# Kernel optimization log

Hardware: AMD Instinct MI355X
Metric: run time of the kernel (lower is better)

Reference implementation:

```python
import jax, jax.numpy as jnp
import numpy as np

B, P, C = 64, 196, 768   # batch, num_patches, hidden_size
HS = 384                 # hidden_s (token-mixing hidden dim)
NG = 8                   # num_grids
GMIN, GMAX = -1.0, 1.0


def _rbf(x):
    # fast-KAN radial basis: exp(-((x - grid_i)/denom)^2), grid over [GMIN, GMAX]
    grid = jnp.linspace(GMIN, GMAX, NG).astype(x.dtype)
    denom = (GMAX - GMIN) / (NG - 1)
    return jnp.exp(-jnp.square((x[..., None] - grid) / denom))  # [..., din, NG]


def _kan_linear(x, spline_w, base_w, base_b):
    # x: [..., din]; spline_w: [dout, din*NG]; base_w: [dout, din]; base_b: [dout]
    basis = _rbf(x).reshape(*x.shape[:-1], -1)          # [..., din*NG]
    out = basis @ spline_w.T                            # spline term (no bias)
    out = out + jax.nn.silu(x) @ base_w.T + base_b      # base update term
    return out


def setup_inputs() -> dict:
    key = jax.random.key(0)
    ks = jax.random.split(key, 5)
    s = 0.1  # spline_weight_init_scale
    return {
        "x": jax.random.normal(ks[0], (B, P, C), jnp.float32),
        "fc1_spline_w": jax.random.normal(ks[1], (HS, P * NG), jnp.float32) * (s / np.sqrt(P * NG)),
        "fc1_base_w": jax.random.normal(ks[2], (HS, P), jnp.float32) / np.sqrt(P),
        "fc1_base_b": jnp.zeros((HS,), jnp.float32),
        "fc2_spline_w": jax.random.normal(ks[3], (P, HS * NG), jnp.float32) * (s / np.sqrt(HS * NG)),
        "fc2_base_w": jax.random.normal(ks[4], (P, HS), jnp.float32) / np.sqrt(HS),
        "fc2_base_b": jnp.zeros((P,), jnp.float32),
    }


def reference(x, fc1_spline_w, fc1_base_w, fc1_base_b,
              fc2_spline_w, fc2_base_w, fc2_base_b):
    skip_param = 1.0
    # token mixing: permute so KANLinear acts over the patch axis
    h = jnp.swapaxes(x, 1, 2)                                   # [B, C, P]
    h = _kan_linear(h, fc1_spline_w, fc1_base_w, fc1_base_b)    # [B, C, HS]
    # dropout p=0 -> identity; the two intermediate permutes cancel
    h = _kan_linear(h, fc2_spline_w, fc2_base_w, fc2_base_b)    # [B, C, P]
    out = jnp.swapaxes(h, 1, 2)                                 # [B, P, C]
    return out + skip_param * x
```

## Files before the change

### kernel.cpp

```cpp
#include <hip/hip_runtime.h>
#include <cstdint>

#define B_  64
#define P_  196
#define C_  768
#define HS_ 384
#define M_  49152
#define RT_ 96
#define NB_ (M_ / RT_)

#define NC1 13
#define KT1 111
#define NT1 12
#define NC2 24
#define KT2 216
#define NT2 7

#define H1_ELEMS  ((size_t)M_ * HS_)
#define W1P_ELEMS ((size_t)KT1 * NT1 * 512)
#define W2P_ELEMS ((size_t)KT2 * NT2 * 512)

typedef __attribute__((ext_vector_type(8)))  short short8;
typedef __attribute__((ext_vector_type(16))) float f32x16;

#define MFMA(w, a, c) __builtin_amdgcn_mfma_f32_32x32x16_bf16((w), (a), (c), 0, 0, 0)

static __device__ __forceinline__ float bf2f(unsigned short u) {
    union { unsigned int i; float f; } v; v.i = ((unsigned int)u) << 16; return v.f;
}
static __device__ __forceinline__ unsigned short f2bf_rne(float f) {
    union { float f; unsigned int i; } v; v.f = f;
    unsigned int r = v.i + 0x7FFFu + ((v.i >> 16) & 1u);
    return (unsigned short)(r >> 16);
}
static __device__ __forceinline__ unsigned int pack2(float a, float b) {
    unsigned int ua = __float_as_uint(a) + 0x8000u;
    unsigned int ub = __float_as_uint(b) + 0x8000u;
    return __builtin_amdgcn_perm(ub, ua, 0x07060302u);
}
static __device__ __forceinline__ short8 rbf8(float s) {
    const float Rr = 1.2011224087864498f;
    const float Aa = 4.2039284307525743f;
    float t1 = __builtin_fmaf(Aa, s, Aa);
    union { short8 s8; unsigned int u[4]; } r;
#pragma unroll
    for (int q = 0; q < 4; q++) {
        float u0 = t1 - (float)(2 * q) * Rr;
        float u1 = t1 - (float)(2 * q + 1) * Rr;
        r.u[q] = pack2(__builtin_amdgcn_exp2f(-u0 * u0),
                       __builtin_amdgcn_exp2f(-u1 * u1));
    }
    return r.s8;
}
static __device__ __forceinline__ unsigned int silu2(float a, float b) {
    const float L2E = 1.4426950408889634f;
    float fa = a * __builtin_amdgcn_rcpf(1.f + __builtin_amdgcn_exp2f(-L2E * a));
    float fb = b * __builtin_amdgcn_rcpf(1.f + __builtin_amdgcn_exp2f(-L2E * b));
    return pack2(fa, fb);
}

__global__ void pack_w_kernel(const float* __restrict__ w1s,
                              const float* __restrict__ w1b,
                              const float* __restrict__ w2s,
                              const float* __restrict__ w2b,
                              unsigned short* __restrict__ w1p,
                              unsigned short* __restrict__ w2p) {
    size_t idx = (size_t)blockIdx.x * 256 + threadIdx.x;
    if (idx < W1P_ELEMS) {
        int j    = idx & 7;
        int lane = (idx >> 3) & 63;
        int lin  = idx >> 9;
        int nt   = lin % NT1;
        int tt   = lin / NT1;
        int cc   = (tt < 108) ? tt / 9 : 12;
        int kk   = (tt < 108) ? tt % 9 : (tt - 108);
        int ktl  = (cc < 12) ? kk : ((kk < 2) ? kk : 8);
        int n = nt * 32 + (lane & 31);
        int khalf = lane >> 5;
        float v = 0.f;
        if (ktl < 8) {
            int p = cc * 16 + ktl * 2 + khalf;
            if (p < P_) v = w1s[(size_t)n * 1568 + p * 8 + j];
        } else {
            int p = cc * 16 + khalf * 8 + j;
            if (p < P_) v = w1b[(size_t)n * 196 + p];
        }
        w1p[idx] = f2bf_rne(v);
    } else {
        size_t idx2 = idx - W1P_ELEMS;
        if (idx2 < W2P_ELEMS) {
            int j    = idx2 & 7;
            int lane = (idx2 >> 3) & 63;
            int lin  = idx2 >> 9;
            int nt   = lin % NT2;
            int tt   = lin / NT2;
            int cc   = tt / 9;
            int ktl  = tt % 9;
            int n = nt * 32 + (lane & 31);
            int khalf = lane >> 5;
            float v = 0.f;
            if (n < P_) {
                if (ktl < 8) {
                    int s = cc * 16 + ktl * 2 + khalf;
                    v = w2s[(size_t)n * 3072 + s * 8 + j];
                } else {
                    int s = cc * 16 + khalf * 8 + j;
                    v = w2b[(size_t)n * 384 + s];
                }
            }
            w2p[idx2] = f2bf_rne(v);
        }
    }
}

#define TS_  1536
#define FB_  (9 * TS_)


__global__ __launch_bounds__(256, 2)
void fc1_kernel(const float* __restrict__ x,
                const unsigned short* __restrict__ w1p,
                const float* __restrict__ b1,
                unsigned short* __restrict__ h1t) {
    __shared__ __align__(16) unsigned short frag[2 * FB_];
    int blk = blockIdx.x;
    int tid = threadIdx.x;
    int b   = blk >> 3;
    int c0  = (blk & 7) * RT_;
    const float* xb = x + (size_t)b * (P_ * C_);

    int colA = tid & 63, scA = tid >> 6;
    int colB = 64 + (tid & 31), scB = tid >> 5;
    int pbase_rbfA  = ((colA >> 5) << 9) + (colA & 31) * 8;
    int pbase_rbfB  = 1024 + (colB & 31) * 8;
    int pbase_siluA = 8 * TS_ + ((colA >> 5) << 9) + ((scA >> 1) << 8) + (colA & 31) * 8 + (scA & 1) * 4;
    int pbase_siluB = 8 * TS_ + 1024 + ((scB >> 2) << 8) + (colB & 31) * 8 + (scB & 3) * 2;

    int wave = tid >> 6, lane = tid & 63;
    int l31 = lane & 31, half = lane >> 5;
    int nt0 = wave * 3;

    f32x16 acc[3][3];
#pragma unroll
    for (int rt = 0; rt < 3; rt++)
#pragma unroll
        for (int nt = 0; nt < 3; nt++)
#pragma unroll
            for (int i = 0; i < 16; i++) acc[rt][nt][i] = 0.f;

    const short8* wp = (const short8*)w1p;
    short8 wbuf[2][3];

    auto wload = [&](int d, const short8* wt0, int kk) {
        const short8* wt = wt0 + (size_t)kk * (NT1 * 64);
        wbuf[d][0] = wt[0]; wbuf[d][1] = wt[64]; wbuf[d][2] = wt[128];
    };
    auto do_mfma = [&](short8 w0, short8 w1, short8 w2,
                       short8 a0, short8 a1, short8 a2) {
        acc[0][0] = MFMA(w0, a0, acc[0][0]); acc[1][0] = MFMA(w0, a1, acc[1][0]); acc[2][0] = MFMA(w0, a2, acc[2][0]);
        acc[0][1] = MFMA(w1, a0, acc[0][1]); acc[1][1] = MFMA(w1, a1, acc[1][1]); acc[2][1] = MFMA(w1, a2, acc[2][1]);
        acc[0][2] = MFMA(w2, a0, acc[0][2]); acc[1][2] = MFMA(w2, a1, acc[1][2]); acc[2][2] = MFMA(w2, a2, acc[2][2]);
    };
    auto produce = [&](int fb, const float (&ra)[4], const float (&rb2)[2]) {
#pragma unroll
        for (int i = 0; i < 4; i++) {
            int sl = scA * 4 + i;
            *(short8*)&frag[fb + (sl >> 1) * TS_ + ((sl & 1) << 8) + pbase_rbfA] = rbf8(ra[i]);
        }
#pragma unroll
        for (int i = 0; i < 2; i++) {
            int sl = scB * 2 + i;
            *(short8*)&frag[fb + (sl >> 1) * TS_ + ((sl & 1) << 8) + pbase_rbfB] = rbf8(rb2[i]);
        }
        uint2 sv;
        sv.x = silu2(ra[0], ra[1]);
        sv.y = silu2(ra[2], ra[3]);
        *(uint2*)&frag[fb + pbase_siluA] = sv;
        *(unsigned int*)&frag[fb + pbase_siluB] = silu2(rb2[0], rb2[1]);
    };
    auto body = [&](int cc, const float (&rbPA)[4], const float (&rbPB)[2],
                    float (&rbLA)[4], float (&rbLB)[2]) {
        const short8* wt0 = wp + ((size_t)(cc * 9) * NT1 + nt0) * 64 + lane;
        wload(0, wt0, 0); wload(1, wt0, 1);
        int fbP = ((cc + 1) & 1) * FB_;
        const unsigned short* fg = &frag[(cc & 1) * FB_];
        short8 a0 = *(const short8*)&fg[lane * 8];
        short8 a1 = *(const short8*)&fg[512 + lane * 8];
        short8 a2 = *(const short8*)&fg[1024 + lane * 8];
#pragma unroll
        for (int kk = 0; kk < 9; kk++) {
            short8 na0, na1, na2;
            if (kk < 8) {
                na0 = *(const short8*)&fg[(kk + 1) * TS_ + lane * 8];
                na1 = *(const short8*)&fg[(kk + 1) * TS_ + 512 + lane * 8];
                na2 = *(const short8*)&fg[(kk + 1) * TS_ + 1024 + lane * 8];
            }
            short8 w0 = wbuf[kk & 1][0], w1 = wbuf[kk & 1][1], w2 = wbuf[kk & 1][2];
            if (kk < 7) wload(kk & 1, wt0, kk + 2);
            if (kk < 4) {
                int sl = scA * 4 + kk;
                *(short8*)&frag[fbP + (sl >> 1) * TS_ + ((sl & 1) << 8) + pbase_rbfA] = rbf8(rbPA[kk]);
            } else if (kk == 4) {
#pragma unroll
                for (int i = 0; i < 2; i++) {
                    int sl = scB * 2 + i;
                    *(short8*)&frag[fbP + (sl >> 1) * TS_ + ((sl & 1) << 8) + pbase_rbfB] = rbf8(rbPB[i]);
                }
            } else if (kk == 5) {
                uint2 sv;
                sv.x = silu2(rbPA[0], rbPA[1]);
                sv.y = silu2(rbPA[2], rbPA[3]);
                *(uint2*)&frag[fbP + pbase_siluA] = sv;
                *(unsigned int*)&frag[fbP + pbase_siluB] = silu2(rbPB[0], rbPB[1]);
            } else if (kk == 6) {
#pragma unroll
                for (int i = 0; i < 2; i++) {
                    int p = (cc + 2) * 16 + scA * 4 + i;
                    p = (p < P_) ? p : (P_ - 1);
                    rbLA[i] = xb[(size_t)p * C_ + c0 + colA];
                }
            } else if (kk == 7) {
#pragma unroll
                for (int i = 2; i < 4; i++) {
                    int p = (cc + 2) * 16 + scA * 4 + i;
                    p = (p < P_) ? p : (P_ - 1);
                    rbLA[i] = xb[(size_t)p * C_ + c0 + colA];
                }
            } else {
#pragma unroll
                for (int i = 0; i < 2; i++) {
                    int p = (cc + 2) * 16 + scB * 2 + i;
                    p = (p < P_) ? p : (P_ - 1);
                    rbLB[i] = xb[(size_t)p * C_ + c0 + colB];
                }
            }
            do_mfma(w0, w1, w2, a0, a1, a2);
            if (kk < 8) { a0 = na0; a1 = na1; a2 = na2; }
        }
        __syncthreads();
    };

    float rbA_A[4], rbB_A[4], rbA_B[2], rbB_B[2];
#pragma unroll
    for (int i = 0; i < 4; i++) {
        rbA_A[i] = xb[(size_t)(scA * 4 + i) * C_ + c0 + colA];
        rbB_A[i] = xb[(size_t)(16 + scA * 4 + i) * C_ + c0 + colA];
    }
#pragma unroll
    for (int i = 0; i < 2; i++) {
        rbA_B[i] = xb[(size_t)(scB * 2 + i) * C_ + c0 + colB];
        rbB_B[i] = xb[(size_t)(16 + scB * 2 + i) * C_ + c0 + colB];
    }
    produce(0, rbA_A, rbA_B);
    __syncthreads();

    for (int c2 = 0; c2 < 6; c2++) {
        body(2 * c2,     rbB_A, rbB_B, rbA_A, rbA_B);
        body(2 * c2 + 1, rbA_A, rbA_B, rbB_A, rbB_B);
    }
    {
        const short8* wt0 = wp + ((size_t)108 * NT1 + nt0) * 64 + lane;
        wload(0, wt0, 0); wload(1, wt0, 1);
        const unsigned short* fg = &frag[0];
#pragma unroll
        for (int kk = 0; kk < 3; kk++) {
            short8 w0 = wbuf[kk & 1][0], w1 = wbuf[kk & 1][1], w2 = wbuf[kk & 1][2];
            if (kk == 0) wload(0, wt0, 2);
            int ktl = (kk < 2) ? kk : 8;
            short8 a0 = *(const short8*)&fg[ktl * TS_ + lane * 8];
            short8 a1 = *(const short8*)&fg[ktl * TS_ + 512 + lane * 8];
            short8 a2 = *(const short8*)&fg[ktl * TS_ + 1024 + lane * 8];
            do_mfma(w0, w1, w2, a0, a1, a2);
        }
    }

#pragma unroll
    for (int nt = 0; nt < 3; nt++) {
        int n0 = (nt0 + nt) * 32 + 4 * half;
#pragma unroll
        for (int reg = 0; reg < 16; reg++) {
            int n = n0 + (reg & 3) + 8 * (reg >> 2);
            float bv = b1[n];
#pragma unroll
            for (int rt = 0; rt < 3; rt++) {
                h1t[(size_t)n * M_ + blk * RT_ + rt * 32 + l31] = f2bf_rne(acc[rt][nt][reg] + bv);
            }
        }
    }
}

__global__ __launch_bounds__(256, 2)
void fc2_kernel(const unsigned short* __restrict__ h1t,
                const unsigned short* __restrict__ w2p,
                const float* __restrict__ b2,
                const float* __restrict__ x,
                float* __restrict__ out) {
    __shared__ __align__(16) unsigned short frag[2 * FB_];
    int blk = blockIdx.x;
    int tid = threadIdx.x;
    int rbase = blk * RT_;

    int colA = tid & 63, scA = tid >> 6;
    int colB = 64 + (tid & 31), scB = tid >> 5;
    int pbase_rbfA  = ((colA >> 5) << 9) + (colA & 31) * 8;
    int pbase_rbfB  = 1024 + (colB & 31) * 8;
    int pbase_siluA = 8 * TS_ + ((colA >> 5) << 9) + ((scA >> 1) << 8) + (colA & 31) * 8 + (scA & 1) * 4;
    int pbase_siluB = 8 * TS_ + 1024 + ((scB >> 2) << 8) + (colB & 31) * 8 + (scB & 3) * 2;

    int wave = tid >> 6, lane = tid & 63;
    int l31 = lane & 31, half = lane >> 5;
    int nt0 = wave * 2;
    int ntn = (wave < 3) ? 2 : 1;
    int off1 = (ntn > 1) ? 64 : 0;

    f32x16 acc[3][2];
#pragma unroll
    for (int rt = 0; rt < 3; rt++)
#pragma unroll
        for (int nt = 0; nt < 2; nt++)
#pragma unroll
            for (int i = 0; i < 16; i++) acc[rt][nt][i] = 0.f;

    const short8* wp = (const short8*)w2p;
    short8 wbuf[2][2];

    auto wload = [&](int d, const short8* wt0, int kk) {
        const short8* wt = wt0 + (size_t)kk * (NT2 * 64);
        wbuf[d][0] = wt[0]; wbuf[d][1] = wt[off1];
    };
    auto do_mfma = [&](short8 w0, short8 w1, short8 a0, short8 a1, short8 a2) {
        acc[0][0] = MFMA(w0, a0, acc[0][0]); acc[1][0] = MFMA(w0, a1, acc[1][0]); acc[2][0] = MFMA(w0, a2, acc[2][0]);
        if (ntn == 2) {
            acc[0][1] = MFMA(w1, a0, acc[0][1]); acc[1][1] = MFMA(w1, a1, acc[1][1]); acc[2][1] = MFMA(w1, a2, acc[2][1]);
        }
    };
    auto produce = [&](int fb, const unsigned short (&ra)[4], const unsigned short (&rb2)[2]) {
        float v0 = bf2f(ra[0]), v1 = bf2f(ra[1]), v2 = bf2f(ra[2]), v3 = bf2f(ra[3]);
        float u0 = bf2f(rb2[0]), u1 = bf2f(rb2[1]);
        float vv[4] = {v0, v1, v2, v3};
#pragma unroll
        for (int i = 0; i < 4; i++) {
            int sl = scA * 4 + i;
            *(short8*)&frag[fb + (sl >> 1) * TS_ + ((sl & 1) << 8) + pbase_rbfA] = rbf8(vv[i]);
        }
        float uu[2] = {u0, u1};
#pragma unroll
        for (int i = 0; i < 2; i++) {
            int sl = scB * 2 + i;
            *(short8*)&frag[fb + (sl >> 1) * TS_ + ((sl & 1) << 8) + pbase_rbfB] = rbf8(uu[i]);
        }
        uint2 sv;
        sv.x = silu2(v0, v1);
        sv.y = silu2(v2, v3);
        *(uint2*)&frag[fb + pbase_siluA] = sv;
        *(unsigned int*)&frag[fb + pbase_siluB] = silu2(u0, u1);
    };
    auto body = [&](int cc, const unsigned short (&rbPA)[4], const unsigned short (&rbPB)[2],
                    unsigned short (&rbLA)[4], unsigned short (&rbLB)[2]) {
        bool doProd = (cc + 1 < NC2);
        const short8* wt0 = wp + ((size_t)(cc * 9) * NT2 + nt0) * 64 + lane;
        wload(0, wt0, 0); wload(1, wt0, 1);
        int fbP = ((cc + 1) & 1) * FB_;
        const unsigned short* fg = &frag[(cc & 1) * FB_];
        short8 a0 = *(const short8*)&fg[lane * 8];
        short8 a1 = *(const short8*)&fg[512 + lane * 8];
        short8 a2 = *(const short8*)&fg[1024 + lane * 8];
#pragma unroll
        for (int kk = 0; kk < 9; kk++) {
            short8 na0, na1, na2;
            if (kk < 8) {
                na0 = *(const short8*)&fg[(kk + 1) * TS_ + lane * 8];
                na1 = *(const short8*)&fg[(kk + 1) * TS_ + 512 + lane * 8];
                na2 = *(const short8*)&fg[(kk + 1) * TS_ + 1024 + lane * 8];
            }
            short8 w0 = wbuf[kk & 1][0], w1 = wbuf[kk & 1][1];
            if (kk < 7) wload(kk & 1, wt0, kk + 2);
            if (kk < 4) {
                if (doProd) {
                    int sl = scA * 4 + kk;
                    *(short8*)&frag[fbP + (sl >> 1) * TS_ + ((sl & 1) << 8) + pbase_rbfA] =
                        rbf8(bf2f(rbPA[kk]));
                }
            } else if (kk == 4) {
                if (doProd) {
#pragma unroll
                    for (int i = 0; i < 2; i++) {
                        int sl = scB * 2 + i;
                        *(short8*)&frag[fbP + (sl >> 1) * TS_ + ((sl & 1) << 8) + pbase_rbfB] =
                            rbf8(bf2f(rbPB[i]));
                    }
                }
            } else if (kk == 5) {
                if (doProd) {
                    uint2 sv;
                    sv.x = silu2(bf2f(rbPA[0]), bf2f(rbPA[1]));
                    sv.y = silu2(bf2f(rbPA[2]), bf2f(rbPA[3]));
                    *(uint2*)&frag[fbP + pbase_siluA] = sv;
                    *(unsigned int*)&frag[fbP + pbase_siluB] = silu2(bf2f(rbPB[0]), bf2f(rbPB[1]));
                }
            } else if (kk == 6) {
#pragma unroll
                for (int i = 0; i < 2; i++) {
                    int s = (cc + 2) * 16 + scA * 4 + i;
                    s = (s < HS_) ? s : (HS_ - 1);
                    rbLA[i] = h1t[(size_t)s * M_ + rbase + colA];
                }
            } else if (kk == 7) {
#pragma unroll
                for (int i = 2; i < 4; i++) {
                    int s = (cc + 2) * 16 + scA * 4 + i;
                    s = (s < HS_) ? s : (HS_ - 1);
                    rbLA[i] = h1t[(size_t)s * M_ + rbase + colA];
                }
            } else {
#pragma unroll
                for (int i = 0; i < 2; i++) {
                    int s = (cc + 2) * 16 + scB * 2 + i;
                    s = (s < HS_) ? s : (HS_ - 1);
                    rbLB[i] = h1t[(size_t)s * M_ + rbase + colB];
                }
            }
            do_mfma(w0, w1, a0, a1, a2);
            if (kk < 8) { a0 = na0; a1 = na1; a2 = na2; }
        }
        __syncthreads();
    };

    unsigned short rbA_A[4], rbB_A[4], rbA_B[2], rbB_B[2];
#pragma unroll
    for (int i = 0; i < 4; i++) {
        rbA_A[i] = h1t[(size_t)(scA * 4 + i) * M_ + rbase + colA];
        rbB_A[i] = h1t[(size_t)(16 + scA * 4 + i) * M_ + rbase + colA];
    }
#pragma unroll
    for (int i = 0; i < 2; i++) {
        rbA_B[i] = h1t[(size_t)(scB * 2 + i) * M_ + rbase + colB];
        rbB_B[i] = h1t[(size_t)(16 + scB * 2 + i) * M_ + rbase + colB];
    }
    produce(0, rbA_A, rbA_B);
    __syncthreads();

    for (int c2 = 0; c2 < 12; c2++) {
        body(2 * c2,     rbB_A, rbB_B, rbA_A, rbA_B);
        body(2 * c2 + 1, rbA_A, rbA_B, rbB_A, rbB_B);
    }

    int b = blk >> 3;
    int c0 = (blk & 7) * RT_;
#pragma unroll
    for (int nt = 0; nt < 2; nt++) {
        if (nt < ntn) {
            int p0 = (nt0 + nt) * 32 + 4 * half;
#pragma unroll
            for (int reg = 0; reg < 16; reg++) {
                int p = p0 + (reg & 3) + 8 * (reg >> 2);
                if (p < P_) {
                    float bv = b2[p];
#pragma unroll
                    for (int rt = 0; rt < 3; rt++) {
                        size_t off = ((size_t)b * P_ + p) * C_ + c0 + rt * 32 + l31;
                        out[off] = acc[rt][nt][reg] + bv + x[off];
                    }
                }
            }
        }
    }
}

extern "C" void kernel_launch(void* const* d_in, const int* in_sizes, int n_in,
                              void* d_out, int out_size, void* d_ws, size_t ws_size,
                              hipStream_t stream) {
    const float* x   = (const float*)d_in[0];
    const float* w1s = (const float*)d_in[1];
    const float* w1b = (const float*)d_in[2];
    const float* b1  = (const float*)d_in[3];
    const float* w2s = (const float*)d_in[4];
    const float* w2b = (const float*)d_in[5];
    const float* b2  = (const float*)d_in[6];
    float* out = (float*)d_out;

    unsigned short* h1t = (unsigned short*)d_ws;
    unsigned short* w1p = h1t + H1_ELEMS;
    unsigned short* w2p = w1p + W1P_ELEMS;

    int pack_blocks = (int)((W1P_ELEMS + W2P_ELEMS) / 256);
    pack_w_kernel<<<pack_blocks, 256, 0, stream>>>(w1s, w1b, w2s, w2b, w1p, w2p);
    fc1_kernel<<<NB_, 256, 0, stream>>>(x, w1p, b1, h1t);
    fc2_kernel<<<NB_, 256, 0, stream>>>(h1t, w2p, b2, x, out);
}
```

Before: 248.5 us.

## Build RBF/SiLU MFMA operands in registers instead of via LDS staging

Both KAN GEMM kernels drop the shared-memory fragment buffers and the per-chunk __syncthreads. Each wave now loads the x/h1 values it needs straight from global memory and computes the RBF and SiLU bf16 operands in registers, right before each MFMA. This removes LDS writes and reads and the block barriers. In exchange, every wave recomputes the basis for all row tiles instead of sharing that work across the block, which raises redundant global loads and VALU work. fc1 also gives up its cross-chunk prefetch of x, since it now loads x at the start of each chunk.

```diff
diff --git a/kernel.cpp b/kernel.cpp
--- a/kernel.cpp
+++ b/kernel.cpp
@@ -113,31 +113,21 @@
     }
 }
 
-#define TS_  1536
-#define FB_  (9 * TS_)
-
 
 __global__ __launch_bounds__(256, 2)
 void fc1_kernel(const float* __restrict__ x,
                 const unsigned short* __restrict__ w1p,
                 const float* __restrict__ b1,
                 unsigned short* __restrict__ h1t) {
-    __shared__ __align__(16) unsigned short frag[2 * FB_];
     int blk = blockIdx.x;
     int tid = threadIdx.x;
     int b   = blk >> 3;
     int c0  = (blk & 7) * RT_;
     const float* xb = x + (size_t)b * (P_ * C_);
 
-    int colA = tid & 63, scA = tid >> 6;
-    int colB = 64 + (tid & 31), scB = tid >> 5;
-    int pbase_rbfA  = ((colA >> 5) << 9) + (colA & 31) * 8;
-    int pbase_rbfB  = 1024 + (colB & 31) * 8;
-    int pbase_siluA = 8 * TS_ + ((colA >> 5) << 9) + ((scA >> 1) << 8) + (colA & 31) * 8 + (scA & 1) * 4;
-    int pbase_siluB = 8 * TS_ + 1024 + ((scB >> 2) << 8) + (colB & 31) * 8 + (scB & 3) * 2;
-
     int wave = tid >> 6, lane = tid & 63;
-    int l31 = lane & 31, half = lane >> 5;
+    int l31 = lane & 31, khalf = lane >> 5;
+    int half = khalf;
     int nt0 = wave * 3;
 
     f32x16 acc[3][3];
@@ -147,9 +137,13 @@
         for (int nt = 0; nt < 3; nt++)
 #pragma unroll
             for (int i = 0; i < 16; i++) acc[rt][nt][i] = 0.f;
+
+    const float* pr0 = xb + (size_t)khalf * C_ + c0 + l31;
+    const float* pm0 = xb + (size_t)(1 + 7 * khalf) * C_ + c0 + l31;
 
     const short8* wp = (const short8*)w1p;
     short8 wbuf[2][3];
+    float xr[3][8], xm[3][4];
 
     auto wload = [&](int d, const short8* wt0, int kk) {
         const short8* wt = wt0 + (size_t)kk * (NT1 * 64);
@@ -161,116 +155,81 @@
         acc[0][1] = MFMA(w1, a0, acc[0][1]); acc[1][1] = MFMA(w1, a1, acc[1][1]); acc[2][1] = MFMA(w1, a2, acc[2][1]);
         acc[0][2] = MFMA(w2, a0, acc[0][2]); acc[1][2] = MFMA(w2, a1, acc[1][2]); acc[2][2] = MFMA(w2, a2, acc[2][2]);
     };
-    auto produce = [&](int fb, const float (&ra)[4], const float (&rb2)[2]) {
-#pragma unroll
-        for (int i = 0; i < 4; i++) {
-            int sl = scA * 4 + i;
-            *(short8*)&frag[fb + (sl >> 1) * TS_ + ((sl & 1) << 8) + pbase_rbfA] = rbf8(ra[i]);
-        }
-#pragma unroll
-        for (int i = 0; i < 2; i++) {
-            int sl = scB * 2 + i;
-            *(short8*)&frag[fb + (sl >> 1) * TS_ + ((sl & 1) << 8) + pbase_rbfB] = rbf8(rb2[i]);
-        }
-        uint2 sv;
-        sv.x = silu2(ra[0], ra[1]);
-        sv.y = silu2(ra[2], ra[3]);
-        *(uint2*)&frag[fb + pbase_siluA] = sv;
-        *(unsigned int*)&frag[fb + pbase_siluB] = silu2(rb2[0], rb2[1]);
-    };
-    auto body = [&](int cc, const float (&rbPA)[4], const float (&rbPB)[2],
-                    float (&rbLA)[4], float (&rbLB)[2]) {
+    auto loadx = [&](int cc) {
+#pragma unroll
+        for (int rt = 0; rt < 3; rt++) {
+            const float* r = pr0 + rt * 32;
+            const float* m = pm0 + rt * 32;
+#pragma unroll
+            for (int i = 0; i < 8; i++) xr[rt][i] = r[(size_t)(cc * 16 + 2 * i) * C_];
+#pragma unroll
+            for (int i = 0; i < 4; i++) xm[rt][i] = m[(size_t)(cc * 16 + 2 * i) * C_];
+        }
+    };
+    auto mk_rbf = [&](int kk, short8 (&a)[3]) {
+#pragma unroll
+        for (int rt = 0; rt < 3; rt++) a[rt] = rbf8(xr[rt][kk]);
+    };
+    auto mk_silu = [&](short8 (&a)[3]) {
+#pragma unroll
+        for (int rt = 0; rt < 3; rt++) {
+            union { short8 s8; unsigned int u[4]; } r;
+#pragma unroll
+            for (int q = 0; q < 4; q++) {
+                float v0 = khalf ? xm[rt][q] : xr[rt][q];
+                float v1 = khalf ? xr[rt][4 + q] : xm[rt][q];
+                r.u[q] = silu2(v0, v1);
+            }
+            a[rt] = r.s8;
+        }
+    };
+    auto chunk = [&](int cc) {
+        loadx(cc);
         const short8* wt0 = wp + ((size_t)(cc * 9) * NT1 + nt0) * 64 + lane;
         wload(0, wt0, 0); wload(1, wt0, 1);
-        int fbP = ((cc + 1) & 1) * FB_;
-        const unsigned short* fg = &frag[(cc & 1) * FB_];
-        short8 a0 = *(const short8*)&fg[lane * 8];
-        short8 a1 = *(const short8*)&fg[512 + lane * 8];
-        short8 a2 = *(const short8*)&fg[1024 + lane * 8];
+        short8 a[3];
 #pragma unroll
         for (int kk = 0; kk < 9; kk++) {
-            short8 na0, na1, na2;
-            if (kk < 8) {
-                na0 = *(const short8*)&fg[(kk + 1) * TS_ + lane * 8];
-                na1 = *(const short8*)&fg[(kk + 1) * TS_ + 512 + lane * 8];
-                na2 = *(const short8*)&fg[(kk + 1) * TS_ + 1024 + lane * 8];
-            }
             short8 w0 = wbuf[kk & 1][0], w1 = wbuf[kk & 1][1], w2 = wbuf[kk & 1][2];
             if (kk < 7) wload(kk & 1, wt0, kk + 2);
-            if (kk < 4) {
-                int sl = scA * 4 + kk;
-                *(short8*)&frag[fbP + (sl >> 1) * TS_ + ((sl & 1) << 8) + pbase_rbfA] = rbf8(rbPA[kk]);
-            } else if (kk == 4) {
-#pragma unroll
-                for (int i = 0; i < 2; i++) {
-                    int sl = scB * 2 + i;
-                    *(short8*)&frag[fbP + (sl >> 1) * TS_ + ((sl & 1) << 8) + pbase_rbfB] = rbf8(rbPB[i]);
-                }
-            } else if (kk == 5) {
-                uint2 sv;
-                sv.x = silu2(rbPA[0], rbPA[1]);
-                sv.y = silu2(rbPA[2], rbPA[3]);
-                *(uint2*)&frag[fbP + pbase_siluA] = sv;
-                *(unsigned int*)&frag[fbP + pbase_siluB] = silu2(rbPB[0], rbPB[1]);
-            } else if (kk == 6) {
-#pragma unroll
-                for (int i = 0; i < 2; i++) {
-                    int p = (cc + 2) * 16 + scA * 4 + i;
-                    p = (p < P_) ? p : (P_ - 1);
-                    rbLA[i] = xb[(size_t)p * C_ + c0 + colA];
-                }
-            } else if (kk == 7) {
-#pragma unroll
-                for (int i = 2; i < 4; i++) {
-                    int p = (cc + 2) * 16 + scA * 4 + i;
-                    p = (p < P_) ? p : (P_ - 1);
-                    rbLA[i] = xb[(size_t)p * C_ + c0 + colA];
-                }
-            } else {
-#pragma unroll
-                for (int i = 0; i < 2; i++) {
-                    int p = (cc + 2) * 16 + scB * 2 + i;
-                    p = (p < P_) ? p : (P_ - 1);
-                    rbLB[i] = xb[(size_t)p * C_ + c0 + colB];
-                }
-            }
-            do_mfma(w0, w1, w2, a0, a1, a2);
-            if (kk < 8) { a0 = na0; a1 = na1; a2 = na2; }
-        }
-        __syncthreads();
-    };
-
-    float rbA_A[4], rbB_A[4], rbA_B[2], rbB_B[2];
-#pragma unroll
-    for (int i = 0; i < 4; i++) {
-        rbA_A[i] = xb[(size_t)(scA * 4 + i) * C_ + c0 + colA];
-        rbB_A[i] = xb[(size_t)(16 + scA * 4 + i) * C_ + c0 + colA];
-    }
-#pragma unroll
-    for (int i = 0; i < 2; i++) {
-        rbA_B[i] = xb[(size_t)(scB * 2 + i) * C_ + c0 + colB];
-        rbB_B[i] = xb[(size_t)(16 + scB * 2 + i) * C_ + c0 + colB];
-    }
-    produce(0, rbA_A, rbA_B);
-    __syncthreads();
-
-    for (int c2 = 0; c2 < 6; c2++) {
-        body(2 * c2,     rbB_A, rbB_B, rbA_A, rbA_B);
-        body(2 * c2 + 1, rbA_A, rbA_B, rbB_A, rbB_B);
-    }
+            if (kk < 8) mk_rbf(kk, a); else mk_silu(a);
+            do_mfma(w0, w1, w2, a[0], a[1], a[2]);
+        }
+    };
+
+    for (int cc = 0; cc < 12; cc++) chunk(cc);
+
     {
+        const float* xc = xb + c0 + l31;
+#pragma unroll
+        for (int rt = 0; rt < 3; rt++) {
+#pragma unroll
+            for (int i = 0; i < 8; i++) {
+                int p = 192 + 2 * i + khalf; p = (p < P_) ? p : (P_ - 1);
+                xr[rt][i] = xc[(size_t)p * C_ + rt * 32];
+            }
+#pragma unroll
+            for (int i = 0; i < 4; i++) {
+                int p = 192 + 2 * i + 1 + 7 * khalf; p = (p < P_) ? p : (P_ - 1);
+                xm[rt][i] = xc[(size_t)p * C_ + rt * 32];
+            }
+        }
         const short8* wt0 = wp + ((size_t)108 * NT1 + nt0) * 64 + lane;
         wload(0, wt0, 0); wload(1, wt0, 1);
-        const unsigned short* fg = &frag[0];
-#pragma unroll
-        for (int kk = 0; kk < 3; kk++) {
-            short8 w0 = wbuf[kk & 1][0], w1 = wbuf[kk & 1][1], w2 = wbuf[kk & 1][2];
-            if (kk == 0) wload(0, wt0, 2);
-            int ktl = (kk < 2) ? kk : 8;
-            short8 a0 = *(const short8*)&fg[ktl * TS_ + lane * 8];
-            short8 a1 = *(const short8*)&fg[ktl * TS_ + 512 + lane * 8];
-            short8 a2 = *(const short8*)&fg[ktl * TS_ + 1024 + lane * 8];
-            do_mfma(w0, w1, w2, a0, a1, a2);
+        short8 a[3];
+        {
+            short8 w0 = wbuf[0][0], w1 = wbuf[0][1], w2 = wbuf[0][2];
+            wload(0, wt0, 2);
+            mk_rbf(0, a);
+            do_mfma(w0, w1, w2, a[0], a[1], a[2]);
+        }
+        {
+            mk_rbf(1, a);
+            do_mfma(wbuf[1][0], wbuf[1][1], wbuf[1][2], a[0], a[1], a[2]);
+        }
+        {
+            mk_silu(a);
+            do_mfma(wbuf[0][0], wbuf[0][1], wbuf[0][2], a[0], a[1], a[2]);
         }
     }
 
@@ -295,20 +254,13 @@
                 const float* __restrict__ b2,
                 const float* __restrict__ x,
                 float* __restrict__ out) {
-    __shared__ __align__(16) unsigned short frag[2 * FB_];
     int blk = blockIdx.x;
     int tid = threadIdx.x;
     int rbase = blk * RT_;
 
-    int colA = tid & 63, scA = tid >> 6;
-    int colB = 64 + (tid & 31), scB = tid >> 5;
-    int pbase_rbfA  = ((colA >> 5) << 9) + (colA & 31) * 8;
-    int pbase_rbfB  = 1024 + (colB & 31) * 8;
-    int pbase_siluA = 8 * TS_ + ((colA >> 5) << 9) + ((scA >> 1) << 8) + (colA & 31) * 8 + (scA & 1) * 4;
-    int pbase_siluB = 8 * TS_ + 1024 + ((scB >> 2) << 8) + (colB & 31) * 8 + (scB & 3) * 2;
-
     int wave = tid >> 6, lane = tid & 63;
-    int l31 = lane & 31, half = lane >> 5;
+    int l31 = lane & 31, khalf = lane >> 5;
+    int half = khalf;
     int nt0 = wave * 2;
     int ntn = (wave < 3) ? 2 : 1;
     int off1 = (ntn > 1) ? 64 : 0;
@@ -321,8 +273,12 @@
 #pragma unroll
             for (int i = 0; i < 16; i++) acc[rt][nt][i] = 0.f;
 
+    const unsigned short* qr0 = h1t + (size_t)khalf * M_ + rbase + l31;
+    const unsigned short* qm0 = h1t + (size_t)(1 + 7 * khalf) * M_ + rbase + l31;
+
     const short8* wp = (const short8*)w2p;
     short8 wbuf[2][2];
+    unsigned short xrA[3][8], xmA[3][4], xrB[3][8], xmB[3][4];
 
     auto wload = [&](int d, const short8* wt0, int kk) {
         const short8* wt = wt0 + (size_t)kk * (NT2 * 64);
@@ -334,115 +290,53 @@
             acc[0][1] = MFMA(w1, a0, acc[0][1]); acc[1][1] = MFMA(w1, a1, acc[1][1]); acc[2][1] = MFMA(w1, a2, acc[2][1]);
         }
     };
-    auto produce = [&](int fb, const unsigned short (&ra)[4], const unsigned short (&rb2)[2]) {
-        float v0 = bf2f(ra[0]), v1 = bf2f(ra[1]), v2 = bf2f(ra[2]), v3 = bf2f(ra[3]);
-        float u0 = bf2f(rb2[0]), u1 = bf2f(rb2[1]);
-        float vv[4] = {v0, v1, v2, v3};
-#pragma unroll
-        for (int i = 0; i < 4; i++) {
-            int sl = scA * 4 + i;
-            *(short8*)&frag[fb + (sl >> 1) * TS_ + ((sl & 1) << 8) + pbase_rbfA] = rbf8(vv[i]);
-        }
-        float uu[2] = {u0, u1};
-#pragma unroll
-        for (int i = 0; i < 2; i++) {
-            int sl = scB * 2 + i;
-            *(short8*)&frag[fb + (sl >> 1) * TS_ + ((sl & 1) << 8) + pbase_rbfB] = rbf8(uu[i]);
-        }
-        uint2 sv;
-        sv.x = silu2(v0, v1);
-        sv.y = silu2(v2, v3);
-        *(uint2*)&frag[fb + pbase_siluA] = sv;
-        *(unsigned int*)&frag[fb + pbase_siluB] = silu2(u0, u1);
-    };
-    auto body = [&](int cc, const unsigned short (&rbPA)[4], const unsigned short (&rbPB)[2],
-                    unsigned short (&rbLA)[4], unsigned short (&rbLB)[2]) {
-        bool doProd = (cc + 1 < NC2);
+    auto loadx = [&](int cc, unsigned short (&xr)[3][8], unsigned short (&xm)[3][4]) {
+#pragma unroll
+        for (int rt = 0; rt < 3; rt++) {
+            const unsigned short* r = qr0 + rt * 32;
+            const unsigned short* m = qm0 + rt * 32;
+#pragma unroll
+            for (int i = 0; i < 8; i++) xr[rt][i] = r[(size_t)(cc * 16 + 2 * i) * M_];
+#pragma unroll
+            for (int i = 0; i < 4; i++) xm[rt][i] = m[(size_t)(cc * 16 + 2 * i) * M_];
+        }
+    };
+    auto mk_rbf = [&](int kk, short8 (&a)[3], unsigned short (&xr)[3][8]) {
+#pragma unroll
+        for (int rt = 0; rt < 3; rt++) a[rt] = rbf8(bf2f(xr[rt][kk]));
+    };
+    auto mk_silu = [&](short8 (&a)[3], unsigned short (&xr)[3][8], unsigned short (&xm)[3][4]) {
+#pragma unroll
+        for (int rt = 0; rt < 3; rt++) {
+            union { short8 s8; unsigned int u[4]; } r;
+#pragma unroll
+            for (int q = 0; q < 4; q++) {
+                float v0 = bf2f(khalf ? xm[rt][q] : xr[rt][q]);
+                float v1 = bf2f(khalf ? xr[rt][4 + q] : xm[rt][q]);
+                r.u[q] = silu2(v0, v1);
+            }
+            a[rt] = r.s8;
+        }
+    };
+    auto chunk = [&](int cc, unsigned short (&xr)[3][8], unsigned short (&xm)[3][4],
+                     unsigned short (&nxr)[3][8], unsigned short (&nxm)[3][4]) {
         const short8* wt0 = wp + ((size_t)(cc * 9) * NT2 + nt0) * 64 + lane;
         wload(0, wt0, 0); wload(1, wt0, 1);
-        int fbP = ((cc + 1) & 1) * FB_;
-        const unsigned short* fg = &frag[(cc & 1) * FB_];
-        short8 a0 = *(const short8*)&fg[lane * 8];
-        short8 a1 = *(const short8*)&fg[512 + lane * 8];
-        short8 a2 = *(const short8*)&fg[1024 + lane * 8];
+        if (cc + 1 < NC2) loadx(cc + 1, nxr, nxm);
+        short8 a[3];
 #pragma unroll
         for (int kk = 0; kk < 9; kk++) {
-            short8 na0, na1, na2;
-            if (kk < 8) {
-                na0 = *(const short8*)&fg[(kk + 1) * TS_ + lane * 8];
-                na1 = *(const short8*)&fg[(kk + 1) * TS_ + 512 + lane * 8];
-                na2 = *(const short8*)&fg[(kk + 1) * TS_ + 1024 + lane * 8];
-            }
             short8 w0 = wbuf[kk & 1][0], w1 = wbuf[kk & 1][1];
             if (kk < 7) wload(kk & 1, wt0, kk + 2);
-            if (kk < 4) {
-                if (doProd) {
-                    int sl = scA * 4 + kk;
-                    *(short8*)&frag[fbP + (sl >> 1) * TS_ + ((sl & 1) << 8) + pbase_rbfA] =
-                        rbf8(bf2f(rbPA[kk]));
-                }
-            } else if (kk == 4) {
-                if (doProd) {
-#pragma unroll
-                    for (int i = 0; i < 2; i++) {
-                        int sl = scB * 2 + i;
-                        *(short8*)&frag[fbP + (sl >> 1) * TS_ + ((sl & 1) << 8) + pbase_rbfB] =
-                            rbf8(bf2f(rbPB[i]));
-                    }
-                }
-            } else if (kk == 5) {
-                if (doProd) {
-                    uint2 sv;
-                    sv.x = silu2(bf2f(rbPA[0]), bf2f(rbPA[1]));
-                    sv.y = silu2(bf2f(rbPA[2]), bf2f(rbPA[3]));
-                    *(uint2*)&frag[fbP + pbase_siluA] = sv;
-                    *(unsigned int*)&frag[fbP + pbase_siluB] = silu2(bf2f(rbPB[0]), bf2f(rbPB[1]));
-                }
-            } else if (kk == 6) {
-#pragma unroll
-                for (int i = 0; i < 2; i++) {
-                    int s = (cc + 2) * 16 + scA * 4 + i;
-                    s = (s < HS_) ? s : (HS_ - 1);
-                    rbLA[i] = h1t[(size_t)s * M_ + rbase + colA];
-                }
-            } else if (kk == 7) {
-#pragma unroll
-                for (int i = 2; i < 4; i++) {
-                    int s = (cc + 2) * 16 + scA * 4 + i;
-                    s = (s < HS_) ? s : (HS_ - 1);
-                    rbLA[i] = h1t[(size_t)s * M_ + rbase + colA];
-                }
-            } else {
-#pragma unroll
-                for (int i = 0; i < 2; i++) {
-                    int s = (cc + 2) * 16 + scB * 2 + i;
-                    s = (s < HS_) ? s : (HS_ - 1);
-                    rbLB[i] = h1t[(size_t)s * M_ + rbase + colB];
-                }
-            }
-            do_mfma(w0, w1, a0, a1, a2);
-            if (kk < 8) { a0 = na0; a1 = na1; a2 = na2; }
-        }
-        __syncthreads();
-    };
-
-    unsigned short rbA_A[4], rbB_A[4], rbA_B[2], rbB_B[2];
-#pragma unroll
-    for (int i = 0; i < 4; i++) {
-        rbA_A[i] = h1t[(size_t)(scA * 4 + i) * M_ + rbase + colA];
-        rbB_A[i] = h1t[(size_t)(16 + scA * 4 + i) * M_ + rbase + colA];
-    }
-#pragma unroll
-    for (int i = 0; i < 2; i++) {
-        rbA_B[i] = h1t[(size_t)(scB * 2 + i) * M_ + rbase + colB];
-        rbB_B[i] = h1t[(size_t)(16 + scB * 2 + i) * M_ + rbase + colB];
-    }
-    produce(0, rbA_A, rbA_B);
-    __syncthreads();
-
+            if (kk < 8) mk_rbf(kk, a, xr); else mk_silu(a, xr, xm);
+            do_mfma(w0, w1, a[0], a[1], a[2]);
+        }
+    };
+
+    loadx(0, xrA, xmA);
     for (int c2 = 0; c2 < 12; c2++) {
-        body(2 * c2,     rbB_A, rbB_B, rbA_A, rbA_B);
-        body(2 * c2 + 1, rbA_A, rbA_B, rbB_A, rbB_B);
+        chunk(2 * c2,     xrA, xmA, xrB, xmB);
+        chunk(2 * c2 + 1, xrB, xmB, xrA, xmA);
     }
 
     int b = blk >> 3;
```

After: 337.9 us. 36.0% more time.
